# Performance work log

Measured on AMD Instinct MI355X. Metric: run time of the kernel, lower is better.

The kernel has to match this reference:

```python
import math
import jax, jax.numpy as jnp
import numpy as np


def setup_inputs() -> dict:
    key = jax.random.key(0)
    k1, k2, k3, k4 = jax.random.split(key, 4)
    B, C, H, W = 8, 256, 128, 128
    norm_dim, K = 64, 3
    return {
        "fea": jax.random.normal(k1, (B, C, H, W), dtype=jnp.float32),
        "norm_feat": jax.random.normal(k2, (B, norm_dim, 1, 1), dtype=jnp.float32),
        "mod_w": jax.random.normal(k3, (C, norm_dim, 1, 1), dtype=jnp.float32),
        "mod_b": jnp.zeros((C,), dtype=jnp.float32),
        "weight": jax.random.normal(k4, (1, C, C, K, K), dtype=jnp.float32),
    }


def reference(fea, norm_feat, mod_w, mod_b, weight):
    B, C, H, W = fea.shape
    K = weight.shape[-1]
    scale = 1.0 / math.sqrt(C * K * K)
    # 1x1 modulation conv on (B, norm_dim, 1, 1) -> style (B, C)
    style = jnp.einsum('bdhw,cd->bc', norm_feat, mod_w[:, :, 0, 0]) + mod_b  # (B, C)
    # modulate: (1, C_out, C_in, K, K) * (B, 1, C_in, 1, 1)
    w = scale * weight * style[:, None, :, None, None]  # (B, C, C, K, K)
    demod = jax.lax.rsqrt(jnp.sum(w * w, axis=(2, 3, 4)) + 1e-8)  # (B, C)
    w = w * demod[:, :, None, None, None]
    # grouped-conv trick: groups=B, input (1, B*C, H, W), weight (B*C, C, K, K)
    w = w.reshape(B * C, C, K, K)
    x = fea.reshape(1, B * C, H, W)
    out = jax.lax.conv_general_dilated(
        x, w,
        window_strides=(1, 1),
        padding=[(K // 2, K // 2), (K // 2, K // 2)],
        dimension_numbers=('NCHW', 'OIHW', 'NCHW'),
        feature_group_count=B,
    )
    return out.reshape(B, C, H, W)
```

## Files before the change

kernel.cpp:

```cpp
#include <hip/hip_runtime.h>

typedef unsigned short u16;
typedef unsigned int u32;
typedef short s8v __attribute__((ext_vector_type(8)));
typedef float f16v __attribute__((ext_vector_type(16)));
typedef u32 u32x4 __attribute__((ext_vector_type(4)));

__device__ __forceinline__ u16 f2bf(float f) {
    u32 u = __float_as_uint(f);
    u += 0x7FFFu + ((u >> 16) & 1u);
    return (u16)(u >> 16);
}

__device__ __forceinline__ void async_load16(const u16* g, u16* l) {
    __builtin_amdgcn_global_load_lds(
        (const __attribute__((address_space(1))) u32*)g,
        (__attribute__((address_space(3))) u32*)l,
        16, 0, 0);
}

__global__ void style_kernel(const float* __restrict__ norm_feat,
                             const float* __restrict__ mod_w,
                             const float* __restrict__ mod_b,
                             float* __restrict__ style) {
    __shared__ float nf[64];
    __shared__ float mw[256][65];
    const int b = blockIdx.x;
    const int tid = threadIdx.x;

    if (tid < 64) nf[tid] = norm_feat[b * 64 + tid];
    #pragma unroll
    for (int i = 0; i < 64; ++i) {
        int idx = i * 256 + tid;
        mw[idx >> 6][idx & 63] = mod_w[idx];
    }
    __syncthreads();

    float s = mod_b[tid];
    #pragma unroll 8
    for (int d = 0; d < 64; ++d) s += nf[d] * mw[tid][d];
    style[b * 256 + tid] = s;
}

__global__ void modulate_kernel(const float* __restrict__ style,
                                const float* __restrict__ weight,
                                u16* __restrict__ Wmod) {
    const int co = blockIdx.x;
    const int b  = blockIdx.y;
    const int ci = threadIdx.x;

    __shared__ float red[256];

    const float s = style[b * 256 + ci];

    float w9[9];
    const float* wp = weight + ((size_t)co * 256 + ci) * 9;
    float sq = 0.f;
    #pragma unroll
    for (int t = 0; t < 9; ++t) { w9[t] = wp[t]; sq += w9[t] * w9[t]; }

    red[ci] = sq * s * s;
    __syncthreads();
    for (int off = 128; off > 0; off >>= 1) {
        if (ci < off) red[ci] += red[ci + off];
        __syncthreads();
    }
    const float scale = 1.0f / 48.0f;
    const float demod = rsqrtf(scale * scale * red[0] + 1e-8f);
    const float coef  = scale * s * demod;

    const size_t tile = (((size_t)b * 9 * 8 + (co >> 5)) * 16 + (ci >> 4)) * 512
                      + (size_t)((co & 31) + 32 * ((ci >> 3) & 1)) * 8 + (ci & 7);
    #pragma unroll
    for (int t = 0; t < 9; ++t) {
        Wmod[tile + (size_t)t * 65536] = f2bf(w9[t] * coef);
    }
}

__global__ __launch_bounds__(256) void transpose_kernel(const float* __restrict__ fea,
                                                        u16* __restrict__ feaT) {
    __shared__ float lds_t[64][132];
    const int y  = blockIdx.x;
    const int c0 = blockIdx.y * 64;
    const int b  = blockIdx.z;
    const int tid = threadIdx.x;

    #pragma unroll
    for (int r = 0; r < 8; ++r) {
        int i  = r * 256 + tid;
        int c  = i >> 5;
        int x4 = i & 31;
        float4 v = *(const float4*)&fea[(((size_t)(b * 256 + c0 + c)) * 128 + y) * 128 + x4 * 4];
        *(float4*)&lds_t[c][x4 * 4] = v;
    }
    __syncthreads();
    #pragma unroll
    for (int jj = 0; jj < 4; ++jj) {
        int p   = jj * 256 + tid;
        int x   = p & 127;
        int g   = p >> 7;
        int cb8 = g * 8;
        u32x4 wv;
        #pragma unroll
        for (int k = 0; k < 4; ++k) {
            float f0 = lds_t[cb8 + 2 * k][x];
            float f1 = lds_t[cb8 + 2 * k + 1][x];
            wv[k] = (u32)f2bf(f0) | ((u32)f2bf(f1) << 16);
        }
        int c  = c0 + cb8;
        int ch = c >> 4;
        int cg = (c >> 3) & 1;
        size_t off = (((((size_t)b * 128 + y) * 16 + ch) * 2 + cg) * 128 + x) * 8;
        *(u32x4*)&feaT[off] = wv;
    }
}

__global__ __launch_bounds__(256, 1) void conv_mfma(
        const u16* __restrict__ Wmod,
        const u16* __restrict__ feaT,
        float* __restrict__ out) {
    __shared__ u16 lds[2][8208];

    const int lin = blockIdx.x + 64 * blockIdx.y;
    const int nid = (lin & 7) * 64 + (lin >> 3);
    const int yp  = nid & 63;
    const int b   = nid >> 6;

    const int tid  = threadIdx.x;
    const int lane = tid & 63;
    const int wave = tid >> 6;
    const int mw   = wave & 1;
    const int ywv  = wave >> 1;
    const int l31  = lane & 31;
    const int l5   = lane >> 5;

    const int yw_s   = __builtin_amdgcn_readfirstlane(ywv);
    const int y_out_s = 2 * yp + yw_s;
    const bool rokU[3] = { y_out_s > 0, true, y_out_s < 127 };

    if (tid < 16) { lds[0][8192 + tid] = 0; lds[1][8192 + tid] = 0; }

    int rb[3], bqL[3], bqR[3];
    #pragma unroll
    for (int kh = 0; kh < 3; ++kh) {
        const int rr = ywv + kh;
        const int o  = ((rr * 2 + l5) * 128 + (l31 - 1)) * 8;
        rb[kh]  = o;
        bqL[kh] = (l31 > 0)  ? o : 8192;
        bqR[kh] = (l31 < 31) ? (o + 3 * 256 + 16) : 8192;
    }

    const u16* Abase = Wmod + (size_t)b * 9 * 65536
                            + (size_t)(mw * 4) * 8192 + (size_t)lane * 8;

    auto loadA = [&](int t, int i, int ch) -> s8v {
        return *(const s8v*)(Abase + (size_t)t * 65536 + (size_t)i * 8192 + (size_t)ch * 512);
    };

    auto stage = [&](int buf, int ch) {
        u16* ldsb = &lds[buf][0];
        const int cg = wave >> 1;
        const int xq = wave & 1;
        #pragma unroll
        for (int r = 0; r < 4; ++r) {
            int gy = 2 * yp - 1 + r;
            if ((unsigned)gy < 128u) {
                const u16* g = feaT +
                    (((((size_t)b * 128 + gy) * 16 + ch) * 2 + cg) * 128 + xq * 64) * 8
                    + (size_t)lane * 8;
                async_load16(g, ldsb + ((r * 2 + cg) * 128 + xq * 64) * 8);
            }
        }
    };

    f16v acc[4][4];
    #pragma unroll
    for (int i = 0; i < 4; ++i)
        #pragma unroll
        for (int j = 0; j < 4; ++j) acc[i][j] = (f16v)0.0f;

    s8v fr[3][4];

    stage(0, 0);
    #pragma unroll
    for (int g = 0; g < 3; ++g)
        #pragma unroll
        for (int i = 0; i < 4; ++i) fr[g][i] = loadA(g, i, 0);
    __syncthreads();

    #pragma unroll 1
    for (int ch = 0; ch < 16; ++ch) {
        const u16* basep = &lds[ch & 1][0];

        auto readB = [&](int kh, int kw, int j) -> s8v {
            const u16* p;
            if (j == 0 && kw == 0)      p = basep + bqL[kh];
            else if (j == 3 && kw == 2) p = basep + bqR[kh];
            else                        p = basep + rb[kh] + (j * 256 + kw * 8);
            return *(const s8v*)p;
        };

        s8v bfrE[4], bfrO[4];
        #pragma unroll
        for (int j = 0; j < 4; ++j) bfrE[j] = readB(0, 0, j);

        #pragma unroll
        for (int t = 0; t < 9; ++t) {
            const int kh = t / 3, kw = t % 3;
            const int khn = (t + 1) / 3, kwn = (t + 1) % 3;

            if ((t & 1) == 0) {
                if (t < 8) {
                    #pragma unroll
                    for (int j = 0; j < 4; ++j) bfrO[j] = readB(khn, kwn, j);
                }
                if (rokU[kh]) {
                    __builtin_amdgcn_s_setprio(1);
                    #pragma unroll
                    for (int i = 0; i < 4; ++i)
                        #pragma unroll
                        for (int j = 0; j < 4; ++j)
                            acc[i][j] = __builtin_amdgcn_mfma_f32_32x32x16_bf16(
                                fr[t % 3][i], bfrE[j], acc[i][j], 0, 0, 0);
                    __builtin_amdgcn_s_setprio(0);
                }
            } else {
                #pragma unroll
                for (int j = 0; j < 4; ++j) bfrE[j] = readB(khn, kwn, j);
                if (rokU[kh]) {
                    __builtin_amdgcn_s_setprio(1);
                    #pragma unroll
                    for (int i = 0; i < 4; ++i)
                        #pragma unroll
                        for (int j = 0; j < 4; ++j)
                            acc[i][j] = __builtin_amdgcn_mfma_f32_32x32x16_bf16(
                                fr[t % 3][i], bfrO[j], acc[i][j], 0, 0, 0);
                    __builtin_amdgcn_s_setprio(0);
                }
            }

            if (t == 3 && ch < 15) {
                __builtin_amdgcn_sched_barrier(0);
                stage((ch + 1) & 1, ch + 1);
                __builtin_amdgcn_sched_barrier(0);
            }

            if (t < 6) {
                #pragma unroll
                for (int i = 0; i < 4; ++i) fr[t % 3][i] = loadA(t + 3, i, ch);
            } else if (ch < 15) {
                #pragma unroll
                for (int i = 0; i < 4; ++i) fr[t % 3][i] = loadA(t - 6, i, ch + 1);
            }
        }

        if (ch < 15) {
            asm volatile("s_waitcnt vmcnt(12)" ::: "memory");
            __builtin_amdgcn_sched_barrier(0);
            __builtin_amdgcn_s_barrier();
            __builtin_amdgcn_sched_barrier(0);
        }
    }

    const int y_out = 2 * yp + ywv;
    #pragma unroll
    for (int i = 0; i < 4; ++i) {
        #pragma unroll
        for (int j = 0; j < 4; ++j) {
            #pragma unroll
            for (int reg = 0; reg < 16; ++reg) {
                int co = mw * 128 + i * 32 + (reg & 3) + 8 * (reg >> 2) + 4 * l5;
                int x  = j * 32 + l31;
                out[(((size_t)(b * 256 + co) * 128 + y_out) * 128) + x] = acc[i][j][reg];
            }
        }
    }
}

extern "C" void kernel_launch(void* const* d_in, const int* in_sizes, int n_in,
                              void* d_out, int out_size, void* d_ws, size_t ws_size,
                              hipStream_t stream) {
    const float* fea       = (const float*)d_in[0];
    const float* norm_feat = (const float*)d_in[1];
    const float* mod_w     = (const float*)d_in[2];
    const float* mod_b     = (const float*)d_in[3];
    const float* weight    = (const float*)d_in[4];
    float* out = (float*)d_out;

    u16* Wmod = (u16*)d_ws;
    u16* feaT = (u16*)((char*)d_ws + 9u * 1024u * 1024u);
    float* style = (float*)feaT;

    style_kernel<<<dim3(8), 256, 0, stream>>>(norm_feat, mod_w, mod_b, style);
    modulate_kernel<<<dim3(256, 8), 256, 0, stream>>>(style, weight, Wmod);
    transpose_kernel<<<dim3(128, 4, 8), 256, 0, stream>>>(fea, feaT);
    conv_mfma<<<dim3(64, 8), 256, 0, stream>>>(Wmod, feaT, out);
}
```

Before: 371.9 us.

## Read conv B fragments directly from global and shrink per-block tile to one row

```diff
diff --git a/kernel.cpp b/kernel.cpp
--- a/kernel.cpp
+++ b/kernel.cpp
@@ -10,13 +10,6 @@
     u32 u = __float_as_uint(f);
     u += 0x7FFFu + ((u >> 16) & 1u);
     return (u16)(u >> 16);
-}
-
-__device__ __forceinline__ void async_load16(const u16* g, u16* l) {
-    __builtin_amdgcn_global_load_lds(
-        (const __attribute__((address_space(1))) u32*)g,
-        (__attribute__((address_space(3))) u32*)l,
-        16, 0, 0);
 }
 
 __global__ void style_kernel(const float* __restrict__ norm_feat,
@@ -49,15 +42,20 @@
     const int b  = blockIdx.y;
     const int ci = threadIdx.x;
 
+    __shared__ float wlds[2304];
     __shared__ float red[256];
 
+    const float* wsrc = weight + (size_t)co * 2304;
+    #pragma unroll
+    for (int i = 0; i < 9; ++i) wlds[i * 256 + ci] = wsrc[i * 256 + ci];
+
     const float s = style[b * 256 + ci];
+    __syncthreads();
 
     float w9[9];
-    const float* wp = weight + ((size_t)co * 256 + ci) * 9;
     float sq = 0.f;
     #pragma unroll
-    for (int t = 0; t < 9; ++t) { w9[t] = wp[t]; sq += w9[t] * w9[t]; }
+    for (int t = 0; t < 9; ++t) { w9[t] = wlds[ci * 9 + t]; sq += w9[t] * w9[t]; }
 
     red[ci] = sq * s * s;
     __syncthreads();
@@ -115,89 +113,59 @@
     }
 }
 
-__global__ __launch_bounds__(256, 1) void conv_mfma(
+__global__ __launch_bounds__(256, 2) void conv_mfma(
         const u16* __restrict__ Wmod,
         const u16* __restrict__ feaT,
         float* __restrict__ out) {
-    __shared__ u16 lds[2][8208];
-
-    const int lin = blockIdx.x + 64 * blockIdx.y;
-    const int nid = (lin & 7) * 64 + (lin >> 3);
-    const int yp  = nid & 63;
-    const int b   = nid >> 6;
+    const int lin = blockIdx.x + 128 * blockIdx.y;
+    const int nid = (lin & 7) * 128 + (lin >> 3);
+    const int y   = nid & 127;
+    const int b   = nid >> 7;
 
     const int tid  = threadIdx.x;
     const int lane = tid & 63;
     const int wave = tid >> 6;
-    const int mw   = wave & 1;
-    const int ywv  = wave >> 1;
     const int l31  = lane & 31;
     const int l5   = lane >> 5;
 
-    const int yw_s   = __builtin_amdgcn_readfirstlane(ywv);
-    const int y_out_s = 2 * yp + yw_s;
-    const bool rokU[3] = { y_out_s > 0, true, y_out_s < 127 };
-
-    if (tid < 16) { lds[0][8192 + tid] = 0; lds[1][8192 + tid] = 0; }
-
-    int rb[3], bqL[3], bqR[3];
+    const bool rokU[3] = { y > 0, true, y < 127 };
+    const bool xz0  = (l31 == 0);
+    const bool xz31 = (l31 == 31);
+
+    const u16* Bb[3];
     #pragma unroll
     for (int kh = 0; kh < 3; ++kh) {
-        const int rr = ywv + kh;
-        const int o  = ((rr * 2 + l5) * 128 + (l31 - 1)) * 8;
-        rb[kh]  = o;
-        bqL[kh] = (l31 > 0)  ? o : 8192;
-        bqR[kh] = (l31 < 31) ? (o + 3 * 256 + 16) : 8192;
+        int gy = y - 1 + kh;
+        int gyc = gy < 0 ? 0 : (gy > 127 ? 127 : gy);
+        Bb[kh] = feaT + ((((size_t)(b * 128 + gyc) * 16) * 2 + l5) * 128 + (l31 - 1)) * 8;
     }
 
     const u16* Abase = Wmod + (size_t)b * 9 * 65536
-                            + (size_t)(mw * 4) * 8192 + (size_t)lane * 8;
+                            + (size_t)(wave * 2) * 8192 + (size_t)lane * 8;
 
     auto loadA = [&](int t, int i, int ch) -> s8v {
         return *(const s8v*)(Abase + (size_t)t * 65536 + (size_t)i * 8192 + (size_t)ch * 512);
     };
 
-    auto stage = [&](int buf, int ch) {
-        u16* ldsb = &lds[buf][0];
-        const int cg = wave >> 1;
-        const int xq = wave & 1;
-        #pragma unroll
-        for (int r = 0; r < 4; ++r) {
-            int gy = 2 * yp - 1 + r;
-            if ((unsigned)gy < 128u) {
-                const u16* g = feaT +
-                    (((((size_t)b * 128 + gy) * 16 + ch) * 2 + cg) * 128 + xq * 64) * 8
-                    + (size_t)lane * 8;
-                async_load16(g, ldsb + ((r * 2 + cg) * 128 + xq * 64) * 8);
-            }
-        }
-    };
-
-    f16v acc[4][4];
-    #pragma unroll
-    for (int i = 0; i < 4; ++i)
+    f16v acc[2][4];
+    #pragma unroll
+    for (int i = 0; i < 2; ++i)
         #pragma unroll
         for (int j = 0; j < 4; ++j) acc[i][j] = (f16v)0.0f;
 
-    s8v fr[3][4];
-
-    stage(0, 0);
+    s8v fr[3][2];
     #pragma unroll
     for (int g = 0; g < 3; ++g)
         #pragma unroll
-        for (int i = 0; i < 4; ++i) fr[g][i] = loadA(g, i, 0);
-    __syncthreads();
+        for (int i = 0; i < 2; ++i) fr[g][i] = loadA(g, i, 0);
 
     #pragma unroll 1
     for (int ch = 0; ch < 16; ++ch) {
-        const u16* basep = &lds[ch & 1][0];
-
         auto readB = [&](int kh, int kw, int j) -> s8v {
-            const u16* p;
-            if (j == 0 && kw == 0)      p = basep + bqL[kh];
-            else if (j == 3 && kw == 2) p = basep + bqR[kh];
-            else                        p = basep + rb[kh] + (j * 256 + kw * 8);
-            return *(const s8v*)p;
+            s8v v = *(const s8v*)(Bb[kh] + (j * 32 + kw) * 8);
+            if (kw == 0 && j == 0) { if (xz0)  v = (s8v)0; }
+            if (kw == 2 && j == 3) { if (xz31) v = (s8v)0; }
+            return v;
         };
 
         s8v bfrE[4], bfrO[4];
@@ -206,7 +174,7 @@
 
         #pragma unroll
         for (int t = 0; t < 9; ++t) {
-            const int kh = t / 3, kw = t % 3;
+            const int kh = t / 3;
             const int khn = (t + 1) / 3, kwn = (t + 1) % 3;
 
             if ((t & 1) == 0) {
@@ -215,63 +183,47 @@
                     for (int j = 0; j < 4; ++j) bfrO[j] = readB(khn, kwn, j);
                 }
                 if (rokU[kh]) {
-                    __builtin_amdgcn_s_setprio(1);
                     #pragma unroll
-                    for (int i = 0; i < 4; ++i)
+                    for (int i = 0; i < 2; ++i)
                         #pragma unroll
                         for (int j = 0; j < 4; ++j)
                             acc[i][j] = __builtin_amdgcn_mfma_f32_32x32x16_bf16(
                                 fr[t % 3][i], bfrE[j], acc[i][j], 0, 0, 0);
-                    __builtin_amdgcn_s_setprio(0);
                 }
             } else {
                 #pragma unroll
                 for (int j = 0; j < 4; ++j) bfrE[j] = readB(khn, kwn, j);
                 if (rokU[kh]) {
-                    __builtin_amdgcn_s_setprio(1);
                     #pragma unroll
-                    for (int i = 0; i < 4; ++i)
+                    for (int i = 0; i < 2; ++i)
                         #pragma unroll
                         for (int j = 0; j < 4; ++j)
                             acc[i][j] = __builtin_amdgcn_mfma_f32_32x32x16_bf16(
                                 fr[t % 3][i], bfrO[j], acc[i][j], 0, 0, 0);
-                    __builtin_amdgcn_s_setprio(0);
                 }
             }
 
-            if (t == 3 && ch < 15) {
-                __builtin_amdgcn_sched_barrier(0);
-                stage((ch + 1) & 1, ch + 1);
-                __builtin_amdgcn_sched_barrier(0);
-            }
-
             if (t < 6) {
                 #pragma unroll
-                for (int i = 0; i < 4; ++i) fr[t % 3][i] = loadA(t + 3, i, ch);
+                for (int i = 0; i < 2; ++i) fr[t % 3][i] = loadA(t + 3, i, ch);
             } else if (ch < 15) {
                 #pragma unroll
-                for (int i = 0; i < 4; ++i) fr[t % 3][i] = loadA(t - 6, i, ch + 1);
+                for (int i = 0; i < 2; ++i) fr[t % 3][i] = loadA(t - 6, i, ch + 1);
             }
         }
 
-        if (ch < 15) {
-            asm volatile("s_waitcnt vmcnt(12)" ::: "memory");
-            __builtin_amdgcn_sched_barrier(0);
-            __builtin_amdgcn_s_barrier();
-            __builtin_amdgcn_sched_barrier(0);
-        }
-    }
-
-    const int y_out = 2 * yp + ywv;
-    #pragma unroll
-    for (int i = 0; i < 4; ++i) {
+        Bb[0] += 2048; Bb[1] += 2048; Bb[2] += 2048;
+    }
+
+    #pragma unroll
+    for (int i = 0; i < 2; ++i) {
         #pragma unroll
         for (int j = 0; j < 4; ++j) {
             #pragma unroll
             for (int reg = 0; reg < 16; ++reg) {
-                int co = mw * 128 + i * 32 + (reg & 3) + 8 * (reg >> 2) + 4 * l5;
+                int co = wave * 64 + i * 32 + (reg & 3) + 8 * (reg >> 2) + 4 * l5;
                 int x  = j * 32 + l31;
-                out[(((size_t)(b * 256 + co) * 128 + y_out) * 128) + x] = acc[i][j][reg];
+                out[(((size_t)(b * 256 + co) * 128 + y) * 128) + x] = acc[i][j][reg];
             }
         }
     }
@@ -294,5 +246,5 @@
     style_kernel<<<dim3(8), 256, 0, stream>>>(norm_feat, mod_w, mod_b, style);
     modulate_kernel<<<dim3(256, 8), 256, 0, stream>>>(style, weight, Wmod);
     transpose_kernel<<<dim3(128, 4, 8), 256, 0, stream>>>(fea, feaT);
-    conv_mfma<<<dim3(64, 8), 256, 0, stream>>>(Wmod, feaT, out);
-}
+    conv_mfma<<<dim3(128, 8), 256, 0, stream>>>(Wmod, feaT, out);
+}
```

Measured after the change: 404.2 us. +8.7%, slower.

## Stagger conv channel-chunk order per block, coalesce modulate loads, drop setprio

Applied to the files above, without the earlier changes.

```diff
diff --git a/kernel.cpp b/kernel.cpp
--- a/kernel.cpp
+++ b/kernel.cpp
@@ -49,15 +49,20 @@
     const int b  = blockIdx.y;
     const int ci = threadIdx.x;
 
+    __shared__ float wlds[2304];
     __shared__ float red[256];
 
+    const float* wsrc = weight + (size_t)co * 2304;
+    #pragma unroll
+    for (int i = 0; i < 9; ++i) wlds[i * 256 + ci] = wsrc[i * 256 + ci];
+
     const float s = style[b * 256 + ci];
+    __syncthreads();
 
     float w9[9];
-    const float* wp = weight + ((size_t)co * 256 + ci) * 9;
     float sq = 0.f;
     #pragma unroll
-    for (int t = 0; t < 9; ++t) { w9[t] = wp[t]; sq += w9[t] * w9[t]; }
+    for (int t = 0; t < 9; ++t) { w9[t] = wlds[ci * 9 + t]; sq += w9[t] * w9[t]; }
 
     red[ci] = sq * s * s;
     __syncthreads();
@@ -126,6 +131,8 @@
     const int yp  = nid & 63;
     const int b   = nid >> 6;
 
+    const int phase = ((yp >> 5) & 1) * 8;
+
     const int tid  = threadIdx.x;
     const int lane = tid & 63;
     const int wave = tid >> 6;
@@ -181,16 +188,18 @@
 
     s8v fr[3][4];
 
-    stage(0, 0);
+    stage(0, phase);
     #pragma unroll
     for (int g = 0; g < 3; ++g)
         #pragma unroll
-        for (int i = 0; i < 4; ++i) fr[g][i] = loadA(g, i, 0);
+        for (int i = 0; i < 4; ++i) fr[g][i] = loadA(g, i, phase);
     __syncthreads();
 
     #pragma unroll 1
-    for (int ch = 0; ch < 16; ++ch) {
-        const u16* basep = &lds[ch & 1][0];
+    for (int chi = 0; chi < 16; ++chi) {
+        const int ch  = (chi + phase) & 15;
+        const int chn = (ch + 1) & 15;
+        const u16* basep = &lds[chi & 1][0];
 
         auto readB = [&](int kh, int kw, int j) -> s8v {
             const u16* p;
@@ -206,7 +215,7 @@
 
         #pragma unroll
         for (int t = 0; t < 9; ++t) {
-            const int kh = t / 3, kw = t % 3;
+            const int kh = t / 3;
             const int khn = (t + 1) / 3, kwn = (t + 1) % 3;
 
             if ((t & 1) == 0) {
@@ -215,46 +224,42 @@
                     for (int j = 0; j < 4; ++j) bfrO[j] = readB(khn, kwn, j);
                 }
                 if (rokU[kh]) {
-                    __builtin_amdgcn_s_setprio(1);
                     #pragma unroll
                     for (int i = 0; i < 4; ++i)
                         #pragma unroll
                         for (int j = 0; j < 4; ++j)
                             acc[i][j] = __builtin_amdgcn_mfma_f32_32x32x16_bf16(
                                 fr[t % 3][i], bfrE[j], acc[i][j], 0, 0, 0);
-                    __builtin_amdgcn_s_setprio(0);
                 }
             } else {
                 #pragma unroll
                 for (int j = 0; j < 4; ++j) bfrE[j] = readB(khn, kwn, j);
                 if (rokU[kh]) {
-                    __builtin_amdgcn_s_setprio(1);
                     #pragma unroll
                     for (int i = 0; i < 4; ++i)
                         #pragma unroll
                         for (int j = 0; j < 4; ++j)
                             acc[i][j] = __builtin_amdgcn_mfma_f32_32x32x16_bf16(
                                 fr[t % 3][i], bfrO[j], acc[i][j], 0, 0, 0);
-                    __builtin_amdgcn_s_setprio(0);
                 }
             }
 
-            if (t == 3 && ch < 15) {
+            if (t == 3 && chi < 15) {
                 __builtin_amdgcn_sched_barrier(0);
-                stage((ch + 1) & 1, ch + 1);
+                stage((chi + 1) & 1, chn);
                 __builtin_amdgcn_sched_barrier(0);
             }
 
             if (t < 6) {
                 #pragma unroll
                 for (int i = 0; i < 4; ++i) fr[t % 3][i] = loadA(t + 3, i, ch);
-            } else if (ch < 15) {
+            } else if (chi < 15) {
                 #pragma unroll
-                for (int i = 0; i < 4; ++i) fr[t % 3][i] = loadA(t - 6, i, ch + 1);
-            }
-        }
-
-        if (ch < 15) {
+                for (int i = 0; i < 4; ++i) fr[t % 3][i] = loadA(t - 6, i, chn);
+            }
+        }
+
+        if (chi < 15) {
             asm volatile("s_waitcnt vmcnt(12)" ::: "memory");
             __builtin_amdgcn_sched_barrier(0);
             __builtin_amdgcn_s_barrier();
```

Measured after the change: 369.1 us. No clear change (-0.7%).
